# Performance work log

Measured on AMD Instinct MI355X. Metric: run time of the kernel, lower is better.

## Reference

```python
import jax, jax.numpy as jnp
import numpy as np
import math

D_MODEL = 1024
N_HEAD = 16
HEAD_DIM = D_MODEL // N_HEAD
BATCH = 4
MAX_LEN = 1024


def _shift(BD):
    # BD: (b, h, L, 2L) -> (b, h, L, L), Transformer-XL relative shift
    b, h, L, _ = BD.shape
    zero_pad = jnp.zeros((b, h, L, 1), BD.dtype)
    BD = jnp.concatenate([BD, zero_pad], axis=-1)      # (b,h,L,2L+1)
    BD = BD.reshape(b, h, -1, L)[:, :, :-1]            # (b,h,2L,L)
    BD = BD.reshape(b, h, L, -1)                       # (b,h,L,2L)
    return BD[:, :, :, L:]                             # (b,h,L,L)


def setup_inputs() -> dict:
    key = jax.random.key(0)
    ks = jax.random.split(key, 10)
    s = 1.0 / math.sqrt(D_MODEL)
    return {
        "q": jax.random.normal(ks[0], (BATCH, MAX_LEN, D_MODEL), jnp.float32),
        "k": jax.random.normal(ks[1], (BATCH, MAX_LEN, D_MODEL), jnp.float32),
        "mask": jax.random.randint(ks[2], (BATCH, MAX_LEN), 0, 2, jnp.int32),
        "pos_embed": jax.random.normal(ks[3], (2 * MAX_LEN, HEAD_DIM), jnp.float32),
        "Wq": jax.random.normal(ks[4], (D_MODEL, D_MODEL), jnp.float32) * s,
        "Wkv": jax.random.normal(ks[5], (D_MODEL, 2 * D_MODEL), jnp.float32) * s,
        "Wr": jax.random.normal(ks[6], (HEAD_DIM, HEAD_DIM), jnp.float32) / math.sqrt(HEAD_DIM),
        "r_r_bias": jax.random.normal(ks[7], (N_HEAD, HEAD_DIM), jnp.float32) * 0.02,
        "r_w_bias": jax.random.normal(ks[8], (N_HEAD, HEAD_DIM), jnp.float32) * 0.02,
    }


def reference(q, k, mask, pos_embed, Wq, Wkv, Wr, r_r_bias, r_w_bias):
    B, L, D = q.shape
    H = r_r_bias.shape[0]
    hd = D // H
    scale = math.sqrt(hd)

    r = pos_embed @ Wr                                   # (2L, hd)
    qh = (q @ Wq).reshape(B, L, H, hd).transpose(0, 2, 1, 3)   # (B,H,L,hd)
    kv = k @ Wkv                                         # (B,L,2D)
    kk, vv = jnp.split(kv, 2, axis=-1)
    kh = kk.reshape(B, L, H, hd).transpose(0, 2, 1, 3)
    vh = vv.reshape(B, L, H, hd).transpose(0, 2, 1, 3)

    AC = jnp.einsum('bhqd,bhkd->bhqk', qh + r_r_bias[None, :, None, :], kh)
    BD = jnp.einsum('bhqd,ld->bhql', qh + r_w_bias[None, :, None, :], r)  # (B,H,L,2L)
    BD = _shift(BD)

    attn = (AC + BD) / scale
    attn = jnp.where(mask[:, None, None, :] == 0, -jnp.inf, attn)
    attn = jax.nn.softmax(attn, axis=-1)

    out = jnp.einsum('bhqk,bhkd->bhqd', attn, vh)        # (B,H,L,hd)
    return out.transpose(0, 2, 1, 3).reshape(B, L, D)
```

## Files before the change

### kernel.cpp

```cpp
#include <hip/hip_runtime.h>

typedef short bf16x8 __attribute__((ext_vector_type(8)));
typedef float f32x4 __attribute__((ext_vector_type(4)));
typedef unsigned short u16;
typedef unsigned short u16x4 __attribute__((ext_vector_type(4)));
typedef unsigned short u16x8 __attribute__((ext_vector_type(8)));
typedef unsigned int u32;

#define NB 4
#define LEN 1024
#define DM 1024
#define NH 16
#define HD 64

#define QSCALE 0.18033688011112043f

__device__ __forceinline__ u16 f2bf(float f) {
    union { float f; unsigned u; } v; v.f = f;
    return (u16)((v.u + 0x7fffu + ((v.u >> 16) & 1u)) >> 16);
}

__device__ __forceinline__ float exp2f_fast(float x) {
    float r; asm("v_exp_f32 %0, %1" : "=v"(r) : "v"(x)); return r;
}

__device__ __forceinline__ unsigned cvt_pk_bf16(float a, float b) {
    unsigned r; asm("v_cvt_pk_bf16_f32 %0, %1, %2" : "=v"(r) : "v"(a), "v"(b)); return r;
}

__device__ __forceinline__ f32x4 mfma16(bf16x8 a, bf16x8 b, f32x4 c) {
    return __builtin_amdgcn_mfma_f32_16x16x32_bf16(a, b, c, 0, 0, 0);
}

__device__ __forceinline__ void gload16(const void* g, void* l) {
    __builtin_amdgcn_global_load_lds(
        (const __attribute__((address_space(1))) unsigned int*)g,
        (__attribute__((address_space(3))) unsigned int*)l, 16, 0, 0);
}

__global__ void prep(const float* __restrict__ q, const float* __restrict__ k,
                     const int* __restrict__ msk,
                     const float* __restrict__ Wq, const float* __restrict__ Wkv,
                     const float* __restrict__ pos, const float* __restrict__ Wr,
                     u16* __restrict__ qbf, u16* __restrict__ kbf,
                     u16* __restrict__ WqT, u16* __restrict__ WkvT,
                     u16* __restrict__ rbf, float* __restrict__ mb) {
    __shared__ float tile[32][33];
    const int f = blockIdx.x;
    const int tid = threadIdx.x;
    if (f < 3072) {
        const int x = f % 96, y = f / 96;
        const bool isQ = x < 32;
        const float* W = isQ ? Wq : Wkv;
        u16* WT = isQ ? WqT : WkvT;
        const int N = isQ ? 1024 : 2048;
        const int n0 = (isQ ? x : x - 32) * 32;
        const int k0 = y * 32;
        const int tx = tid & 31, ty = tid >> 5;
        #pragma unroll
        for (int j = 0; j < 4; j++) {
            int r = ty + j * 8;
            tile[r][tx] = W[(size_t)(k0 + r) * N + n0 + tx];
        }
        __syncthreads();
        #pragma unroll
        for (int j = 0; j < 4; j++) {
            int r = ty + j * 8;
            WT[(size_t)(n0 + r) * 1024 + k0 + tx] = f2bf(tile[tx][r]);
        }
    } else if (f < 3588) {
        int idx = (f - 3072) * 256 + tid;
        if (idx < 2064 * 64) {
            int row = idx >> 6, col = idx & 63;
            float s = 0.f;
            if (row < 2048) {
                #pragma unroll
                for (int kk = 0; kk < 64; kk++) s += pos[row * 64 + kk] * Wr[kk * 64 + col];
            }
            const int csw = (((col >> 3) ^ (row & 7)) << 3) | (col & 7);
            rbf[(row << 6) | csw] = f2bf(s);
        }
    } else if (f < 3604) {
        int i = (f - 3588) * 256 + tid;
        if (i < NB * LEN) mb[i] = msk[i] ? 0.f : -3.0e38f;
    } else {
        int idx = (f - 3604) * 256 + tid;
        if (idx < 1048576) {
            float4 v = ((const float4*)q)[idx];
            u16x4 o;
            o[0] = f2bf(v.x); o[1] = f2bf(v.y); o[2] = f2bf(v.z); o[3] = f2bf(v.w);
            ((u16x4*)qbf)[idx] = o;
        } else if (idx < 2097152) {
            int i = idx - 1048576;
            float4 v = ((const float4*)k)[i];
            u16x4 o;
            o[0] = f2bf(v.x); o[1] = f2bf(v.y); o[2] = f2bf(v.z); o[3] = f2bf(v.w);
            ((u16x4*)kbf)[i] = o;
        }
    }
}

__global__ __launch_bounds__(256) void gemm_all(
    const u16* __restrict__ qbf, const u16* __restrict__ kbf,
    const u16* __restrict__ WqT, const u16* __restrict__ WkvT,
    const float* __restrict__ rrb, const float* __restrict__ rwb,
    u16* __restrict__ A1, u16* __restrict__ A2,
    u16* __restrict__ khs, u16* __restrict__ vhsT)
{
    __shared__ u16 as[2][128][32];
    __shared__ u16 bs[2][128][32];

    const int fb = blockIdx.x;
    const int wsw = ((fb & 7) * 96) + (fb >> 3);
    const int bx = wsw % 24;
    const bool isQ = bx < 8;
    const u16* Abf = isQ ? qbf : kbf;
    const u16* BT  = isQ ? WqT : WkvT;
    const int n0 = (isQ ? bx : bx - 8) * 128;
    const int m0 = (wsw / 24) * 128;
    const int tid = threadIdx.x;
    const int w = tid >> 6, lane = tid & 63, g = lane >> 4, c = lane & 15;
    const int wm = w >> 1, wn = w & 1;
    const int srow = lane >> 2, sj = lane & 3;

    const f32x4 fzero = {0.f, 0.f, 0.f, 0.f};
    f32x4 acc[4][4];
    #pragma unroll
    for (int i = 0; i < 4; i++)
        #pragma unroll
        for (int j = 0; j < 4; j++) acc[i][j] = fzero;

    auto STAGE = [&](int buf, int ks) {
        const int k0 = ks * 32;
        #pragma unroll
        for (int i = 0; i < 2; i++) {
            const int rb = w * 32 + i * 16;
            const int rowA = rb + srow;
            gload16(Abf + (size_t)(m0 + rowA) * 1024 + k0 + ((sj ^ (rowA & 3)) << 3),
                    &as[buf][rb][0]);
            gload16(BT + (size_t)(n0 + rowA) * 1024 + k0 + ((sj ^ (rowA & 3)) << 3),
                    &bs[buf][rb][0]);
        }
    };

    STAGE(0, 0);
    __syncthreads();

    for (int ks = 0; ks < 32; ks++) {
        const int cur = ks & 1, nb = cur ^ 1;
        if (ks < 31) STAGE(nb, ks + 1);

        bf16x8 af[4], bfr[4];
        #pragma unroll
        for (int i = 0; i < 4; i++) {
            const int row = wm * 64 + i * 16 + c;
            af[i] = *(const bf16x8*)&as[cur][row][(g ^ (row & 3)) << 3];
        }
        #pragma unroll
        for (int j = 0; j < 4; j++) {
            const int row = wn * 64 + j * 16 + c;
            bfr[j] = *(const bf16x8*)&bs[cur][row][(g ^ (row & 3)) << 3];
        }
        #pragma unroll
        for (int i = 0; i < 4; i++)
            #pragma unroll
            for (int j = 0; j < 4; j++)
                acc[i][j] = mfma16(af[i], bfr[j], acc[i][j]);

        __syncthreads();
    }

    #pragma unroll
    for (int j = 0; j < 4; j++) {
        const int n = n0 + wn * 64 + j * 16 + c;
        float b1v = 0.f, b2v = 0.f;
        if (isQ) { b1v = rrb[n]; b2v = rwb[n]; }
        #pragma unroll
        for (int i = 0; i < 4; i++) {
            const int l0 = m0 + wm * 64 + i * 16 + 4 * g;
            if (!isQ && n >= DM) {
                const int d = n & 63, hh = (n - DM) >> 6;
                const int bb = l0 >> 10, l = l0 & 1023;
                u16x4 o;
                #pragma unroll
                for (int r = 0; r < 4; r++) o[r] = f2bf(acc[i][j][r]);
                *(u16x4*)(vhsT + (((size_t)(bb * NH + hh)) * HD + d) * LEN + l) = o;
            } else {
                #pragma unroll
                for (int r = 0; r < 4; r++) {
                    const int row = l0 + r;
                    const int bb = row >> 10, l = row & 1023;
                    const float v = acc[i][j][r];
                    if (isQ) {
                        size_t idx = (((size_t)(bb * NH + (n >> 6))) * LEN + l) * HD + (n & 63);
                        A1[idx] = f2bf((v + b1v) * QSCALE);
                        A2[idx] = f2bf((v + b2v) * QSCALE);
                    } else {
                        const int d = n & 63;
                        const int dsw = (((d >> 3) ^ (l & 7)) << 3) | (d & 7);
                        size_t idx = (((size_t)(bb * NH + (n >> 6))) * LEN + l) * HD + dsw;
                        khs[idx] = f2bf(v);
                    }
                }
            }
        }
    }
}

__global__ __launch_bounds__(256, 2) void attn_kernel(
    const u16* __restrict__ A1, const u16* __restrict__ A2,
    const u16* __restrict__ khs, const u16* __restrict__ vhsT,
    const u16* __restrict__ rbf, const float* __restrict__ mbias,
    float* __restrict__ outp)
{
    __shared__ u16 kbuf[2][32][64];
    __shared__ u16 rbuf[192][64];
    __shared__ u16 vbuf[2][4][64][8];
    __shared__ float biasl[1024];
    __shared__ float gl[4][2][16][52];
    __shared__ u16 pl[4][32][40];

    const int bh = blockIdx.x;
    const int b = bh >> 4, h = bh & 15;
    const int tid = threadIdx.x;
    const int w = tid >> 6, lane = tid & 63, g = lane >> 4, c = lane & 15;
    const int q0 = blockIdx.y * 128, q0w = q0 + w * 32;
    const int lrow8 = lane >> 3, lcol = lane & 7;
    const int kkey = (c + 1) & 7;

    const u16* Kbase = khs + (size_t)bh * LEN * HD;
    const u16* Vp = vhsT + (size_t)bh * HD * LEN;
    u16* plw = &pl[w][0][0];

    const u16* A1p = A1 + ((size_t)bh * LEN + q0w) * HD;
    const u16* A2p = A2 + ((size_t)bh * LEN + q0w) * HD;
    bf16x8 a1f[2][2], a2f[2][2];
    #pragma unroll
    for (int qs = 0; qs < 2; qs++)
        #pragma unroll
        for (int kf = 0; kf < 2; kf++) {
            a1f[qs][kf] = *(const bf16x8*)(A1p + (qs * 16 + c) * HD + kf * 32 + g * 8);
            a2f[qs][kf] = *(const bf16x8*)(A2p + (qs * 16 + c) * HD + kf * 32 + g * 8);
        }

    gload16(mbias + b * LEN + w * 256 + lane * 4, &biasl[w * 256]);
    gload16(Kbase + (((size_t)(w * 8 + lrow8)) << 6) + (lcol << 3), &kbuf[0][w * 8][0]);
    gload16(Vp + ((size_t)lane << 10) + w * 8, &vbuf[0][w][0][0]);
    const int js0 = LEN - q0 - 128;
    #pragma unroll
    for (int i = 0; i < 5; i++) {
        const int jg = js0 + (w + 4 * i) * 8;
        gload16(rbf + (((size_t)(jg + lrow8)) << 6) + (lcol << 3), &rbuf[jg % 192][0]);
    }
    __syncthreads();

    int psl = (js0 + 160) % 192;
    int bsl = (LEN - q0w - 31) % 192;

    bf16x8 RA[2][2], RB[2][2];
    #pragma unroll
    for (int mt = 0; mt < 2; mt++) {
        int t = bsl + mt * 16 + c; if (t >= 192) t -= 192;
        #pragma unroll
        for (int kf = 0; kf < 2; kf++)
            RA[mt][kf] = *(const bf16x8*)&rbuf[t][((4 * kf + g) ^ kkey) * 8];
    }

    const f32x4 fzero = {0.f, 0.f, 0.f, 0.f};
    f32x4 oacc[2][4];
    #pragma unroll
    for (int qs = 0; qs < 2; qs++)
        #pragma unroll
        for (int dt = 0; dt < 4; dt++) oacc[qs][dt] = fzero;
    float mrow[2] = {-3.0e38f, -3.0e38f}, lrow[2] = {0.f, 0.f};

    auto STEP = [&](int kt, bf16x8 (&Rold)[2][2], bf16x8 (&Rnew)[2][2]) {
        const int cur = kt & 1, nb = cur ^ 1;
        const int c0 = kt * 32;

        if (kt < 31) {
            const int c0n = c0 + 32;
            gload16(Kbase + (((size_t)(c0n + w * 8 + lrow8)) << 6) + (lcol << 3), &kbuf[nb][w * 8][0]);
            gload16(Vp + ((size_t)lane << 10) + c0n + w * 8, &vbuf[nb][w][0][0]);
            const int pg = js0 + 160 + 32 * kt + 8 * w;
            int ps = psl + 8 * w; if (ps >= 192) ps -= 192;
            gload16(rbf + (((size_t)(pg + lrow8)) << 6) + (lcol << 3), &rbuf[ps][0]);
        }

        bf16x8 Kf[2][2];
        #pragma unroll
        for (int ct = 0; ct < 2; ct++)
            #pragma unroll
            for (int kf = 0; kf < 2; kf++)
                Kf[ct][kf] = *(const bf16x8*)&kbuf[cur][16 * ct + c][((4 * kf + g) ^ (c & 7)) * 8];

        bf16x8 Rf[4][2];
        #pragma unroll
        for (int kf = 0; kf < 2; kf++) { Rf[0][kf] = Rold[0][kf]; Rf[1][kf] = Rold[1][kf]; }
        #pragma unroll
        for (int mt = 0; mt < 2; mt++) {
            int t = bsl + 32 + mt * 16 + c; if (t >= 192) t -= 192;
            #pragma unroll
            for (int kf = 0; kf < 2; kf++) {
                Rf[2 + mt][kf] = *(const bf16x8*)&rbuf[t][((4 * kf + g) ^ kkey) * 8];
                Rnew[mt][kf] = Rf[2 + mt][kf];
            }
        }

        __builtin_amdgcn_s_setprio(1);
        f32x4 s[2][2];
        #pragma unroll
        for (int qs = 0; qs < 2; qs++)
            #pragma unroll
            for (int ct = 0; ct < 2; ct++) {
                f32x4 a = fzero;
                a = mfma16(Kf[ct][0], a1f[qs][0], a);
                a = mfma16(Kf[ct][1], a1f[qs][1], a);
                s[qs][ct] = a;
            }
        #pragma unroll
        for (int mt = 1; mt < 4; mt++) {
            f32x4 ga = fzero;
            ga = mfma16(Rf[mt][0], a2f[0][0], ga);
            ga = mfma16(Rf[mt][1], a2f[0][1], ga);
            *(f32x4*)&gl[w][0][c][(mt - 1) * 16 + 4 * g] = ga;
        }
        #pragma unroll
        for (int mt = 0; mt < 3; mt++) {
            f32x4 ga = fzero;
            ga = mfma16(Rf[mt][0], a2f[1][0], ga);
            ga = mfma16(Rf[mt][1], a2f[1][1], ga);
            *(f32x4*)&gl[w][1][c][mt * 16 + 4 * g] = ga;
        }
        __builtin_amdgcn_s_setprio(0);

        const float* glq0 = &gl[w][0][c][0];
        const float* glq1 = &gl[w][1][c][0];
        f32x4 bb0 = *(const f32x4*)&biasl[c0 + 4 * g];
        f32x4 bb1 = *(const f32x4*)&biasl[c0 + 16 + 4 * g];
        #pragma unroll
        for (int r = 0; r < 4; r++) {
            const int gidx = 4 * g + r + 15 - c;
            s[0][0][r] += glq0[gidx] + bb0[r];
            s[0][1][r] += glq0[gidx + 16] + bb1[r];
            s[1][0][r] += glq1[gidx] + bb0[r];
            s[1][1][r] += glq1[gidx + 16] + bb1[r];
        }

        bf16x8 Vb[4];
        #pragma unroll
        for (int dt = 0; dt < 4; dt++)
            Vb[dt] = *(const bf16x8*)&vbuf[cur][g][16 * dt + c][0];

        #pragma unroll
        for (int qs = 0; qs < 2; qs++) {
            float t = fmaxf(fmaxf(fmaxf(s[qs][0][0], s[qs][0][1]), fmaxf(s[qs][0][2], s[qs][0][3])),
                            fmaxf(fmaxf(s[qs][1][0], s[qs][1][1]), fmaxf(s[qs][1][2], s[qs][1][3])));
            t = fmaxf(t, __shfl_xor(t, 16));
            t = fmaxf(t, __shfl_xor(t, 32));
            if (!__all(t <= mrow[qs] + 8.f)) {
                const float mnew = fmaxf(mrow[qs], t);
                const float alpha = exp2f_fast(mrow[qs] - mnew);
                mrow[qs] = mnew;
                lrow[qs] *= alpha;
                #pragma unroll
                for (int dt = 0; dt < 4; dt++)
                    #pragma unroll
                    for (int r = 0; r < 4; r++) oacc[qs][dt][r] *= alpha;
            }
            const float mref = mrow[qs];
            float p[8];
            float ps = 0.f;
            #pragma unroll
            for (int r = 0; r < 4; r++) {
                p[r] = exp2f_fast(s[qs][0][r] - mref);
                p[4 + r] = exp2f_fast(s[qs][1][r] - mref);
                ps += p[r] + p[4 + r];
            }
            lrow[qs] += ps;
            const unsigned d0 = cvt_pk_bf16(p[0], p[1]);
            const unsigned d1 = cvt_pk_bf16(p[2], p[3]);
            const unsigned d2 = cvt_pk_bf16(p[4], p[5]);
            const unsigned d3 = cvt_pk_bf16(p[6], p[7]);
            const int prow = (qs * 16 + c) * 40;
            *(uint2*)&plw[prow + 4 * g] = make_uint2(d0, d1);
            *(uint2*)&plw[prow + 16 + 4 * g] = make_uint2(d2, d3);
            bf16x8 pbr = *(const bf16x8*)&plw[prow + 8 * g];
            __builtin_amdgcn_s_setprio(1);
            #pragma unroll
            for (int dt = 0; dt < 4; dt++)
                oacc[qs][dt] = mfma16(Vb[dt], pbr, oacc[qs][dt]);
            __builtin_amdgcn_s_setprio(0);
        }

        psl += 32; if (psl >= 192) psl -= 192;
        bsl += 32; if (bsl >= 192) bsl -= 192;
        __syncthreads();
    };

    for (int kt2 = 0; kt2 < 16; kt2++) {
        STEP(2 * kt2,     RA, RB);
        STEP(2 * kt2 + 1, RB, RA);
    }

    #pragma unroll
    for (int qs = 0; qs < 2; qs++) {
        float sum = lrow[qs];
        sum += __shfl_xor(sum, 16);
        sum += __shfl_xor(sum, 32);
        const float inv = sum > 0.f ? 1.0f / sum : 0.f;
        const int l = q0w + qs * 16 + c;
        float* op = outp + ((size_t)b * LEN + l) * DM + h * HD;
        #pragma unroll
        for (int dt = 0; dt < 4; dt++) {
            f32x4 o;
            #pragma unroll
            for (int r = 0; r < 4; r++) o[r] = oacc[qs][dt][r] * inv;
            *(f32x4*)(op + dt * 16 + 4 * g) = o;
        }
    }
}

extern "C" void kernel_launch(void* const* d_in, const int* in_sizes, int n_in,
                              void* d_out, int out_size, void* d_ws, size_t ws_size,
                              hipStream_t stream) {
    const float* q   = (const float*)d_in[0];
    const float* k   = (const float*)d_in[1];
    const int*   msk = (const int*)d_in[2];
    const float* pos = (const float*)d_in[3];
    const float* Wq  = (const float*)d_in[4];
    const float* Wkv = (const float*)d_in[5];
    const float* Wr  = (const float*)d_in[6];
    const float* rrb = (const float*)d_in[7];
    const float* rwb = (const float*)d_in[8];
    float* outp = (float*)d_out;
    char* ws = (char*)d_ws;

    u16* qbf  = (u16*)(ws + 0);
    u16* kbf  = (u16*)(ws + 8388608);
    u16* WqT  = (u16*)(ws + 16777216);
    u16* WkvT = (u16*)(ws + 18874368);
    u16* rbf  = (u16*)(ws + 23068672);
    u16* A1   = (u16*)(ws + 23332864);
    u16* A2   = (u16*)(ws + 31721472);
    u16* khs  = (u16*)(ws + 40110080);
    u16* vhsT = (u16*)(ws + 48498688);
    float* mb = (float*)(ws + 56887296);

    prep<<<11796, 256, 0, stream>>>(q, k, msk, Wq, Wkv, pos, Wr, qbf, kbf, WqT, WkvT, rbf, mb);
    gemm_all<<<768, 256, 0, stream>>>(qbf, kbf, WqT, WkvT, rrb, rwb, A1, A2, khs, vhsT);
    attn_kernel<<<dim3(64, 8), 256, 0, stream>>>(A1, A2, khs, vhsT, rbf, mb, outp);
}
```

Before: 118.4 us.

## Software-pipeline attention loop: overlap next tile scores with current softmax-PV

Splits the per-tile step into score computation (QK and positional MFMA plus bias) and softmax/PV stages, then skews them so tile kt+1's scores are computed while tile kt's softmax and PV run. K/R loads are staged one tile ahead and V loads staged separately one tile behind. This aims to hide MFMA latency and exp/shuffle latency behind each other and to give the scheduler more independent work. It costs extra registers for two score buffers and adds a prologue and epilogue.

Result: no change. 117.6 us (-0.7%).

```diff
diff --git a/kernel.cpp b/kernel.cpp
--- a/kernel.cpp
+++ b/kernel.cpp
@@ -245,7 +245,6 @@
 
     gload16(mbias + b * LEN + w * 256 + lane * 4, &biasl[w * 256]);
     gload16(Kbase + (((size_t)(w * 8 + lrow8)) << 6) + (lcol << 3), &kbuf[0][w * 8][0]);
-    gload16(Vp + ((size_t)lane << 10) + w * 8, &vbuf[0][w][0][0]);
     const int js0 = LEN - q0 - 128;
     #pragma unroll
     for (int i = 0; i < 5; i++) {
@@ -254,16 +253,16 @@
     }
     __syncthreads();
 
-    int psl = (js0 + 160) % 192;
-    int bsl = (LEN - q0w - 31) % 192;
-
     bf16x8 RA[2][2], RB[2][2];
-    #pragma unroll
-    for (int mt = 0; mt < 2; mt++) {
-        int t = bsl + mt * 16 + c; if (t >= 192) t -= 192;
-        #pragma unroll
-        for (int kf = 0; kf < 2; kf++)
-            RA[mt][kf] = *(const bf16x8*)&rbuf[t][((4 * kf + g) ^ kkey) * 8];
+    {
+        const int bsl0 = (LEN - q0w - 31) % 192;
+        #pragma unroll
+        for (int mt = 0; mt < 2; mt++) {
+            int t = bsl0 + mt * 16 + c; if (t >= 192) t -= 192;
+            #pragma unroll
+            for (int kf = 0; kf < 2; kf++)
+                RA[mt][kf] = *(const bf16x8*)&rbuf[t][((4 * kf + g) ^ kkey) * 8];
+        }
     }
 
     const f32x4 fzero = {0.f, 0.f, 0.f, 0.f};
@@ -273,19 +272,23 @@
         #pragma unroll
         for (int dt = 0; dt < 4; dt++) oacc[qs][dt] = fzero;
     float mrow[2] = {-3.0e38f, -3.0e38f}, lrow[2] = {0.f, 0.f};
-
-    auto STEP = [&](int kt, bf16x8 (&Rold)[2][2], bf16x8 (&Rnew)[2][2]) {
-        const int cur = kt & 1, nb = cur ^ 1;
+    f32x4 SA[2][2], SB[2][2];
+
+    auto STAGE_KR = [&](int t) {
+        const int c0t = t * 32;
+        gload16(Kbase + (((size_t)(c0t + w * 8 + lrow8)) << 6) + (lcol << 3), &kbuf[t & 1][w * 8][0]);
+        const int pgb = js0 + 160 + 32 * (t - 1);
+        const int ps = pgb % 192 + 8 * w;
+        gload16(rbf + (((size_t)(pgb + 8 * w + lrow8)) << 6) + (lcol << 3), &rbuf[ps][0]);
+    };
+    auto STAGE_V = [&](int t) {
+        gload16(Vp + ((size_t)lane << 10) + t * 32 + w * 8, &vbuf[t & 1][w][0][0]);
+    };
+
+    auto SCORES = [&](int kt, f32x4 (&sN)[2][2], bf16x8 (&Rold)[2][2], bf16x8 (&Rnew)[2][2]) {
+        const int cur = kt & 1;
         const int c0 = kt * 32;
-
-        if (kt < 31) {
-            const int c0n = c0 + 32;
-            gload16(Kbase + (((size_t)(c0n + w * 8 + lrow8)) << 6) + (lcol << 3), &kbuf[nb][w * 8][0]);
-            gload16(Vp + ((size_t)lane << 10) + c0n + w * 8, &vbuf[nb][w][0][0]);
-            const int pg = js0 + 160 + 32 * kt + 8 * w;
-            int ps = psl + 8 * w; if (ps >= 192) ps -= 192;
-            gload16(rbf + (((size_t)(pg + lrow8)) << 6) + (lcol << 3), &rbuf[ps][0]);
-        }
+        const int bslt = (LEN - q0w - 31 + 32 * kt) % 192;
 
         bf16x8 Kf[2][2];
         #pragma unroll
@@ -299,7 +302,7 @@
         for (int kf = 0; kf < 2; kf++) { Rf[0][kf] = Rold[0][kf]; Rf[1][kf] = Rold[1][kf]; }
         #pragma unroll
         for (int mt = 0; mt < 2; mt++) {
-            int t = bsl + 32 + mt * 16 + c; if (t >= 192) t -= 192;
+            int t = bslt + 32 + mt * 16 + c; if (t >= 192) t -= 192;
             #pragma unroll
             for (int kf = 0; kf < 2; kf++) {
                 Rf[2 + mt][kf] = *(const bf16x8*)&rbuf[t][((4 * kf + g) ^ kkey) * 8];
@@ -308,7 +311,6 @@
         }
 
         __builtin_amdgcn_s_setprio(1);
-        f32x4 s[2][2];
         #pragma unroll
         for (int qs = 0; qs < 2; qs++)
             #pragma unroll
@@ -316,7 +318,7 @@
                 f32x4 a = fzero;
                 a = mfma16(Kf[ct][0], a1f[qs][0], a);
                 a = mfma16(Kf[ct][1], a1f[qs][1], a);
-                s[qs][ct] = a;
+                sN[qs][ct] = a;
             }
         #pragma unroll
         for (int mt = 1; mt < 4; mt++) {
@@ -341,21 +343,24 @@
         #pragma unroll
         for (int r = 0; r < 4; r++) {
             const int gidx = 4 * g + r + 15 - c;
-            s[0][0][r] += glq0[gidx] + bb0[r];
-            s[0][1][r] += glq0[gidx + 16] + bb1[r];
-            s[1][0][r] += glq1[gidx] + bb0[r];
-            s[1][1][r] += glq1[gidx + 16] + bb1[r];
-        }
-
+            sN[0][0][r] += glq0[gidx] + bb0[r];
+            sN[0][1][r] += glq0[gidx + 16] + bb1[r];
+            sN[1][0][r] += glq1[gidx] + bb0[r];
+            sN[1][1][r] += glq1[gidx + 16] + bb1[r];
+        }
+    };
+
+    auto SOFTPV = [&](int kt, f32x4 (&sO)[2][2]) {
+        const int vs = kt & 1;
         bf16x8 Vb[4];
         #pragma unroll
         for (int dt = 0; dt < 4; dt++)
-            Vb[dt] = *(const bf16x8*)&vbuf[cur][g][16 * dt + c][0];
+            Vb[dt] = *(const bf16x8*)&vbuf[vs][g][16 * dt + c][0];
 
         #pragma unroll
         for (int qs = 0; qs < 2; qs++) {
-            float t = fmaxf(fmaxf(fmaxf(s[qs][0][0], s[qs][0][1]), fmaxf(s[qs][0][2], s[qs][0][3])),
-                            fmaxf(fmaxf(s[qs][1][0], s[qs][1][1]), fmaxf(s[qs][1][2], s[qs][1][3])));
+            float t = fmaxf(fmaxf(fmaxf(sO[qs][0][0], sO[qs][0][1]), fmaxf(sO[qs][0][2], sO[qs][0][3])),
+                            fmaxf(fmaxf(sO[qs][1][0], sO[qs][1][1]), fmaxf(sO[qs][1][2], sO[qs][1][3])));
             t = fmaxf(t, __shfl_xor(t, 16));
             t = fmaxf(t, __shfl_xor(t, 32));
             if (!__all(t <= mrow[qs] + 8.f)) {
@@ -373,8 +378,8 @@
             float ps = 0.f;
             #pragma unroll
             for (int r = 0; r < 4; r++) {
-                p[r] = exp2f_fast(s[qs][0][r] - mref);
-                p[4 + r] = exp2f_fast(s[qs][1][r] - mref);
+                p[r] = exp2f_fast(sO[qs][0][r] - mref);
+                p[4 + r] = exp2f_fast(sO[qs][1][r] - mref);
                 ps += p[r] + p[4 + r];
             }
             lrow[qs] += ps;
@@ -392,16 +397,32 @@
                 oacc[qs][dt] = mfma16(Vb[dt], pbr, oacc[qs][dt]);
             __builtin_amdgcn_s_setprio(0);
         }
-
-        psl += 32; if (psl >= 192) psl -= 192;
-        bsl += 32; if (bsl >= 192) bsl -= 192;
+    };
+
+    STAGE_KR(1);
+    STAGE_V(0);
+    SCORES(0, SA, RA, RB);
+    __syncthreads();
+
+    for (int kt2 = 0; kt2 < 15; kt2++) {
+        const int kt = 2 * kt2 + 1;
+        STAGE_KR(kt + 1);
+        STAGE_V(kt);
+        SCORES(kt, SB, RB, RA);
+        SOFTPV(kt - 1, SA);
         __syncthreads();
-    };
-
-    for (int kt2 = 0; kt2 < 16; kt2++) {
-        STEP(2 * kt2,     RA, RB);
-        STEP(2 * kt2 + 1, RB, RA);
-    }
+        STAGE_KR(kt + 2);
+        STAGE_V(kt + 1);
+        SCORES(kt + 1, SA, RA, RB);
+        SOFTPV(kt, SB);
+        __syncthreads();
+    }
+
+    STAGE_V(31);
+    SCORES(31, SB, RB, RA);
+    SOFTPV(30, SA);
+    __syncthreads();
+    SOFTPV(31, SB);
 
     #pragma unroll
     for (int qs = 0; qs < 2; qs++) {
```

## Split attention block into eight waves of 16 query rows each

Applied to the files above, without the earlier changes.

Doubles the attention block to 512 threads, so each wave handles 16 query rows instead of 32. Loads are split across waves: the first four fetch K/V tiles and the others fetch positional-embedding rows. Register carry-over of R fragments between steps is dropped, and all three R fragments are re-read from LDS every step. This should cut register pressure and add waves for latency hiding, but shared K/V tiles are now reused by fewer rows per wave, which means more LDS reads and MFMA issue overhead per FLOP.

Result: no change. 117.1 us (-1.1%).

```diff
diff --git a/kernel.cpp b/kernel.cpp
--- a/kernel.cpp
+++ b/kernel.cpp
@@ -207,7 +207,7 @@
     }
 }
 
-__global__ __launch_bounds__(256, 2) void attn_kernel(
+__global__ __launch_bounds__(512, 4) void attn_kernel(
     const u16* __restrict__ A1, const u16* __restrict__ A2,
     const u16* __restrict__ khs, const u16* __restrict__ vhsT,
     const u16* __restrict__ rbf, const float* __restrict__ mbias,
@@ -217,74 +217,66 @@
     __shared__ u16 rbuf[192][64];
     __shared__ u16 vbuf[2][4][64][8];
     __shared__ float biasl[1024];
-    __shared__ float gl[4][2][16][52];
-    __shared__ u16 pl[4][32][40];
+    __shared__ float gl[8][16][52];
+    __shared__ u16 pl[8][16][40];
 
     const int bh = blockIdx.x;
     const int b = bh >> 4, h = bh & 15;
     const int tid = threadIdx.x;
     const int w = tid >> 6, lane = tid & 63, g = lane >> 4, c = lane & 15;
-    const int q0 = blockIdx.y * 128, q0w = q0 + w * 32;
+    const int q0 = blockIdx.y * 128, q0w = q0 + w * 16;
     const int lrow8 = lane >> 3, lcol = lane & 7;
     const int kkey = (c + 1) & 7;
 
     const u16* Kbase = khs + (size_t)bh * LEN * HD;
     const u16* Vp = vhsT + (size_t)bh * HD * LEN;
     u16* plw = &pl[w][0][0];
+    float* glw = &gl[w][0][0];
 
     const u16* A1p = A1 + ((size_t)bh * LEN + q0w) * HD;
     const u16* A2p = A2 + ((size_t)bh * LEN + q0w) * HD;
-    bf16x8 a1f[2][2], a2f[2][2];
-    #pragma unroll
-    for (int qs = 0; qs < 2; qs++)
-        #pragma unroll
-        for (int kf = 0; kf < 2; kf++) {
-            a1f[qs][kf] = *(const bf16x8*)(A1p + (qs * 16 + c) * HD + kf * 32 + g * 8);
-            a2f[qs][kf] = *(const bf16x8*)(A2p + (qs * 16 + c) * HD + kf * 32 + g * 8);
-        }
-
-    gload16(mbias + b * LEN + w * 256 + lane * 4, &biasl[w * 256]);
-    gload16(Kbase + (((size_t)(w * 8 + lrow8)) << 6) + (lcol << 3), &kbuf[0][w * 8][0]);
-    gload16(Vp + ((size_t)lane << 10) + w * 8, &vbuf[0][w][0][0]);
+    bf16x8 a1f[2], a2f[2];
+    #pragma unroll
+    for (int kf = 0; kf < 2; kf++) {
+        a1f[kf] = *(const bf16x8*)(A1p + c * HD + kf * 32 + g * 8);
+        a2f[kf] = *(const bf16x8*)(A2p + c * HD + kf * 32 + g * 8);
+    }
+
     const int js0 = LEN - q0 - 128;
-    #pragma unroll
-    for (int i = 0; i < 5; i++) {
-        const int jg = js0 + (w + 4 * i) * 8;
-        gload16(rbf + (((size_t)(jg + lrow8)) << 6) + (lcol << 3), &rbuf[jg % 192][0]);
+    if (w < 4) {
+        gload16(Kbase + (((size_t)(8 * w + lrow8)) << 6) + (lcol << 3), &kbuf[0][8 * w][0]);
+        gload16(Vp + ((size_t)lane << 10) + 8 * w, &vbuf[0][w][0][0]);
+        const int gr = 16 + w;
+        gload16(rbf + (((size_t)(js0 + 8 * gr + lrow8)) << 6) + (lcol << 3), &rbuf[(js0 + 8 * gr) % 192][0]);
+    } else {
+        gload16(mbias + b * LEN + (w - 4) * 256 + lane * 4, &biasl[(w - 4) * 256]);
+    }
+    #pragma unroll
+    for (int i = 0; i < 2; i++) {
+        const int gr = w + 8 * i;
+        gload16(rbf + (((size_t)(js0 + 8 * gr + lrow8)) << 6) + (lcol << 3), &rbuf[(js0 + 8 * gr) % 192][0]);
     }
     __syncthreads();
 
-    int psl = (js0 + 160) % 192;
-    int bsl = (LEN - q0w - 31) % 192;
-
-    bf16x8 RA[2][2], RB[2][2];
-    #pragma unroll
-    for (int mt = 0; mt < 2; mt++) {
-        int t = bsl + mt * 16 + c; if (t >= 192) t -= 192;
-        #pragma unroll
-        for (int kf = 0; kf < 2; kf++)
-            RA[mt][kf] = *(const bf16x8*)&rbuf[t][((4 * kf + g) ^ kkey) * 8];
-    }
-
     const f32x4 fzero = {0.f, 0.f, 0.f, 0.f};
-    f32x4 oacc[2][4];
-    #pragma unroll
-    for (int qs = 0; qs < 2; qs++)
-        #pragma unroll
-        for (int dt = 0; dt < 4; dt++) oacc[qs][dt] = fzero;
-    float mrow[2] = {-3.0e38f, -3.0e38f}, lrow[2] = {0.f, 0.f};
-
-    auto STEP = [&](int kt, bf16x8 (&Rold)[2][2], bf16x8 (&Rnew)[2][2]) {
+    f32x4 oacc[4];
+    #pragma unroll
+    for (int dt = 0; dt < 4; dt++) oacc[dt] = fzero;
+    float mrow = -3.0e38f, lrow = 0.f;
+
+    for (int kt = 0; kt < 32; kt++) {
         const int cur = kt & 1, nb = cur ^ 1;
         const int c0 = kt * 32;
 
         if (kt < 31) {
             const int c0n = c0 + 32;
-            gload16(Kbase + (((size_t)(c0n + w * 8 + lrow8)) << 6) + (lcol << 3), &kbuf[nb][w * 8][0]);
-            gload16(Vp + ((size_t)lane << 10) + c0n + w * 8, &vbuf[nb][w][0][0]);
-            const int pg = js0 + 160 + 32 * kt + 8 * w;
-            int ps = psl + 8 * w; if (ps >= 192) ps -= 192;
-            gload16(rbf + (((size_t)(pg + lrow8)) << 6) + (lcol << 3), &rbuf[ps][0]);
+            if (w < 4) {
+                gload16(Kbase + (((size_t)(c0n + 8 * w + lrow8)) << 6) + (lcol << 3), &kbuf[nb][8 * w][0]);
+                gload16(Vp + ((size_t)lane << 10) + c0n + 8 * w, &vbuf[nb][w][0][0]);
+            } else {
+                const int row0 = js0 + 160 + 32 * kt + 8 * (w - 4);
+                gload16(rbf + (((size_t)(row0 + lrow8)) << 6) + (lcol << 3), &rbuf[row0 % 192][0]);
+            }
         }
 
         bf16x8 Kf[2][2];
@@ -294,130 +286,101 @@
             for (int kf = 0; kf < 2; kf++)
                 Kf[ct][kf] = *(const bf16x8*)&kbuf[cur][16 * ct + c][((4 * kf + g) ^ (c & 7)) * 8];
 
-        bf16x8 Rf[4][2];
-        #pragma unroll
-        for (int kf = 0; kf < 2; kf++) { Rf[0][kf] = Rold[0][kf]; Rf[1][kf] = Rold[1][kf]; }
-        #pragma unroll
-        for (int mt = 0; mt < 2; mt++) {
-            int t = bsl + 32 + mt * 16 + c; if (t >= 192) t -= 192;
+        const int bs = (1009 - q0w + 32 * kt) % 192;
+        bf16x8 Rf[3][2];
+        #pragma unroll
+        for (int mt = 0; mt < 3; mt++) {
+            int t = bs + mt * 16 + c; if (t >= 192) t -= 192;
             #pragma unroll
-            for (int kf = 0; kf < 2; kf++) {
-                Rf[2 + mt][kf] = *(const bf16x8*)&rbuf[t][((4 * kf + g) ^ kkey) * 8];
-                Rnew[mt][kf] = Rf[2 + mt][kf];
-            }
+            for (int kf = 0; kf < 2; kf++)
+                Rf[mt][kf] = *(const bf16x8*)&rbuf[t][((4 * kf + g) ^ kkey) * 8];
         }
 
         __builtin_amdgcn_s_setprio(1);
-        f32x4 s[2][2];
-        #pragma unroll
-        for (int qs = 0; qs < 2; qs++)
-            #pragma unroll
-            for (int ct = 0; ct < 2; ct++) {
-                f32x4 a = fzero;
-                a = mfma16(Kf[ct][0], a1f[qs][0], a);
-                a = mfma16(Kf[ct][1], a1f[qs][1], a);
-                s[qs][ct] = a;
-            }
-        #pragma unroll
-        for (int mt = 1; mt < 4; mt++) {
-            f32x4 ga = fzero;
-            ga = mfma16(Rf[mt][0], a2f[0][0], ga);
-            ga = mfma16(Rf[mt][1], a2f[0][1], ga);
-            *(f32x4*)&gl[w][0][c][(mt - 1) * 16 + 4 * g] = ga;
-        }
-        #pragma unroll
-        for (int mt = 0; mt < 3; mt++) {
-            f32x4 ga = fzero;
-            ga = mfma16(Rf[mt][0], a2f[1][0], ga);
-            ga = mfma16(Rf[mt][1], a2f[1][1], ga);
-            *(f32x4*)&gl[w][1][c][mt * 16 + 4 * g] = ga;
-        }
+        f32x4 s0 = fzero, s1 = fzero;
+        s0 = mfma16(Kf[0][0], a1f[0], s0);
+        s0 = mfma16(Kf[0][1], a1f[1], s0);
+        s1 = mfma16(Kf[1][0], a1f[0], s1);
+        s1 = mfma16(Kf[1][1], a1f[1], s1);
+        f32x4 g0 = fzero, g1 = fzero, g2 = fzero;
+        g0 = mfma16(Rf[0][0], a2f[0], g0);
+        g0 = mfma16(Rf[0][1], a2f[1], g0);
+        *(f32x4*)&glw[c * 52 + 4 * g] = g0;
+        g1 = mfma16(Rf[1][0], a2f[0], g1);
+        g1 = mfma16(Rf[1][1], a2f[1], g1);
+        *(f32x4*)&glw[c * 52 + 16 + 4 * g] = g1;
+        g2 = mfma16(Rf[2][0], a2f[0], g2);
+        g2 = mfma16(Rf[2][1], a2f[1], g2);
+        *(f32x4*)&glw[c * 52 + 32 + 4 * g] = g2;
         __builtin_amdgcn_s_setprio(0);
 
-        const float* glq0 = &gl[w][0][c][0];
-        const float* glq1 = &gl[w][1][c][0];
+        const float* glq = &glw[c * 52];
         f32x4 bb0 = *(const f32x4*)&biasl[c0 + 4 * g];
         f32x4 bb1 = *(const f32x4*)&biasl[c0 + 16 + 4 * g];
         #pragma unroll
         for (int r = 0; r < 4; r++) {
             const int gidx = 4 * g + r + 15 - c;
-            s[0][0][r] += glq0[gidx] + bb0[r];
-            s[0][1][r] += glq0[gidx + 16] + bb1[r];
-            s[1][0][r] += glq1[gidx] + bb0[r];
-            s[1][1][r] += glq1[gidx + 16] + bb1[r];
-        }
+            s0[r] += glq[gidx] + bb0[r];
+            s1[r] += glq[gidx + 16] + bb1[r];
+        }
+
+        float t = fmaxf(fmaxf(fmaxf(s0[0], s0[1]), fmaxf(s0[2], s0[3])),
+                        fmaxf(fmaxf(s1[0], s1[1]), fmaxf(s1[2], s1[3])));
+        t = fmaxf(t, __shfl_xor(t, 16));
+        t = fmaxf(t, __shfl_xor(t, 32));
+        if (!__all(t <= mrow + 8.f)) {
+            const float mnew = fmaxf(mrow, t);
+            const float alpha = exp2f_fast(mrow - mnew);
+            mrow = mnew;
+            lrow *= alpha;
+            #pragma unroll
+            for (int dt = 0; dt < 4; dt++)
+                #pragma unroll
+                for (int r = 0; r < 4; r++) oacc[dt][r] *= alpha;
+        }
+        float p[8];
+        float ps = 0.f;
+        #pragma unroll
+        for (int r = 0; r < 4; r++) {
+            p[r] = exp2f_fast(s0[r] - mrow);
+            p[4 + r] = exp2f_fast(s1[r] - mrow);
+            ps += p[r] + p[4 + r];
+        }
+        lrow += ps;
+        const unsigned d0 = cvt_pk_bf16(p[0], p[1]);
+        const unsigned d1 = cvt_pk_bf16(p[2], p[3]);
+        const unsigned d2 = cvt_pk_bf16(p[4], p[5]);
+        const unsigned d3 = cvt_pk_bf16(p[6], p[7]);
+        const int prow = c * 40;
+        *(uint2*)&plw[prow + 4 * g] = make_uint2(d0, d1);
+        *(uint2*)&plw[prow + 16 + 4 * g] = make_uint2(d2, d3);
+        bf16x8 pbr = *(const bf16x8*)&plw[prow + 8 * g];
 
         bf16x8 Vb[4];
         #pragma unroll
         for (int dt = 0; dt < 4; dt++)
             Vb[dt] = *(const bf16x8*)&vbuf[cur][g][16 * dt + c][0];
-
-        #pragma unroll
-        for (int qs = 0; qs < 2; qs++) {
-            float t = fmaxf(fmaxf(fmaxf(s[qs][0][0], s[qs][0][1]), fmaxf(s[qs][0][2], s[qs][0][3])),
-                            fmaxf(fmaxf(s[qs][1][0], s[qs][1][1]), fmaxf(s[qs][1][2], s[qs][1][3])));
-            t = fmaxf(t, __shfl_xor(t, 16));
-            t = fmaxf(t, __shfl_xor(t, 32));
-            if (!__all(t <= mrow[qs] + 8.f)) {
-                const float mnew = fmaxf(mrow[qs], t);
-                const float alpha = exp2f_fast(mrow[qs] - mnew);
-                mrow[qs] = mnew;
-                lrow[qs] *= alpha;
-                #pragma unroll
-                for (int dt = 0; dt < 4; dt++)
-                    #pragma unroll
-                    for (int r = 0; r < 4; r++) oacc[qs][dt][r] *= alpha;
-            }
-            const float mref = mrow[qs];
-            float p[8];
-            float ps = 0.f;
-            #pragma unroll
-            for (int r = 0; r < 4; r++) {
-                p[r] = exp2f_fast(s[qs][0][r] - mref);
-                p[4 + r] = exp2f_fast(s[qs][1][r] - mref);
-                ps += p[r] + p[4 + r];
-            }
-            lrow[qs] += ps;
-            const unsigned d0 = cvt_pk_bf16(p[0], p[1]);
-            const unsigned d1 = cvt_pk_bf16(p[2], p[3]);
-            const unsigned d2 = cvt_pk_bf16(p[4], p[5]);
-            const unsigned d3 = cvt_pk_bf16(p[6], p[7]);
-            const int prow = (qs * 16 + c) * 40;
-            *(uint2*)&plw[prow + 4 * g] = make_uint2(d0, d1);
-            *(uint2*)&plw[prow + 16 + 4 * g] = make_uint2(d2, d3);
-            bf16x8 pbr = *(const bf16x8*)&plw[prow + 8 * g];
-            __builtin_amdgcn_s_setprio(1);
-            #pragma unroll
-            for (int dt = 0; dt < 4; dt++)
-                oacc[qs][dt] = mfma16(Vb[dt], pbr, oacc[qs][dt]);
-            __builtin_amdgcn_s_setprio(0);
-        }
-
-        psl += 32; if (psl >= 192) psl -= 192;
-        bsl += 32; if (bsl >= 192) bsl -= 192;
+        __builtin_amdgcn_s_setprio(1);
+        #pragma unroll
+        for (int dt = 0; dt < 4; dt++)
+            oacc[dt] = mfma16(Vb[dt], pbr, oacc[dt]);
+        __builtin_amdgcn_s_setprio(0);
+
         __syncthreads();
-    };
-
-    for (int kt2 = 0; kt2 < 16; kt2++) {
-        STEP(2 * kt2,     RA, RB);
-        STEP(2 * kt2 + 1, RB, RA);
-    }
-
-    #pragma unroll
-    for (int qs = 0; qs < 2; qs++) {
-        float sum = lrow[qs];
-        sum += __shfl_xor(sum, 16);
-        sum += __shfl_xor(sum, 32);
-        const float inv = sum > 0.f ? 1.0f / sum : 0.f;
-        const int l = q0w + qs * 16 + c;
-        float* op = outp + ((size_t)b * LEN + l) * DM + h * HD;
-        #pragma unroll
-        for (int dt = 0; dt < 4; dt++) {
-            f32x4 o;
-            #pragma unroll
-            for (int r = 0; r < 4; r++) o[r] = oacc[qs][dt][r] * inv;
-            *(f32x4*)(op + dt * 16 + 4 * g) = o;
-        }
+    }
+
+    float sum = lrow;
+    sum += __shfl_xor(sum, 16);
+    sum += __shfl_xor(sum, 32);
+    const float inv = sum > 0.f ? 1.0f / sum : 0.f;
+    const int l = q0w + c;
+    float* op = outp + ((size_t)b * LEN + l) * DM + h * HD;
+    #pragma unroll
+    for (int dt = 0; dt < 4; dt++) {
+        f32x4 o;
+        #pragma unroll
+        for (int r = 0; r < 4; r++) o[r] = oacc[dt][r] * inv;
+        *(f32x4*)(op + dt * 16 + 4 * g) = o;
     }
 }
 
@@ -449,5 +412,5 @@
 
     prep<<<11796, 256, 0, stream>>>(q, k, msk, Wq, Wkv, pos, Wr, qbf, kbf, WqT, WkvT, rbf, mb);
     gemm_all<<<768, 256, 0, stream>>>(qbf, kbf, WqT, WkvT, rrb, rwb, A1, A2, khs, vhsT);
-    attn_kernel<<<dim3(64, 8), 256, 0, stream>>>(A1, A2, khs, vhsT, rbf, mb, outp);
-}
+    attn_kernel<<<dim3(64, 8), 512, 0, stream>>>(A1, A2, khs, vhsT, rbf, mb, outp);
+}
```
